# Optimization experiments

Measured on AMD Instinct MI355X. Metric: run time of the kernel, lower is better.

Reference implementation:

```python
import jax, jax.numpy as jnp
import numpy as np
from math import log2, floor

B, N, DIM = 2, 2048, 2048
HEADS, DIM_HEAD, FF_MULT = 16, 128, 4
RMS_EPS = 1e-8


def _get_slopes(heads):
    def pow2_slopes(n):
        start = 2 ** (-2 ** (-(log2(n) - 3)))
        return [start * start ** i for i in range(n)]
    if log2(heads).is_integer():
        return pow2_slopes(heads)
    closest = 2 ** floor(log2(heads))
    return pow2_slopes(closest) + pow2_slopes(2 * closest)[0::2][: heads - closest]


def setup_inputs() -> dict:
    key = jax.random.key(0)
    ks = jax.random.split(key, 5)
    std = 0.02
    return {
        "x": jax.random.normal(ks[0], (B, N, DIM), dtype=jnp.float32),
        "g": jnp.ones((DIM,), dtype=jnp.float32),
        "w_qkv": jax.random.normal(ks[1], (DIM, DIM + DIM_HEAD), dtype=jnp.float32) * std,
        "w_attn_out": jax.random.normal(ks[2], (DIM, DIM), dtype=jnp.float32) * std,
        "w_ff1": jax.random.normal(ks[3], (DIM, 2 * FF_MULT * DIM), dtype=jnp.float32) * std,
        "w_ff2": jax.random.normal(ks[4], (FF_MULT * DIM, DIM), dtype=jnp.float32) * std,
    }


def reference(x, g, w_qkv, w_attn_out, w_ff1, w_ff2):
    b, n, dim = x.shape
    # RMSNorm: x / clamp(||x|| * dim^-0.5, eps) * g
    norm = jnp.linalg.norm(x, axis=-1, keepdims=True) * (dim ** -0.5)
    xn = x / jnp.maximum(norm, RMS_EPS) * g

    # Parallel SwiGLU FFN branch (shares normed input with attention)
    h = xn @ w_ff1                       # [b, n, 2*ff_mult*dim]
    val, gate = jnp.split(h, 2, axis=-1)
    ff_out = (jax.nn.silu(gate) * val) @ w_ff2  # [b, n, dim]

    # Multi-query attention: single dim_head-wide kv shared as K and V
    qkv = xn @ w_qkv                     # [b, n, dim + dim_head]
    q, kv = qkv[..., :dim], qkv[..., dim:]
    q = q.reshape(b, n, HEADS, DIM_HEAD) * (DIM_HEAD ** -0.5)
    sim = jnp.einsum('bihd,bjd->bhij', q, kv)  # [b, h, n, n]

    # ALiBi bias: -|j - i| * slope_h
    slopes = jnp.asarray(_get_slopes(HEADS), dtype=sim.dtype)[:, None, None]
    pos = jnp.arange(n)
    bias = -jnp.abs(pos[None, None, :] - pos[None, :, None]).astype(sim.dtype) * slopes
    sim = sim + bias

    # Causal mask (strict upper triangle masked)
    causal = jnp.triu(jnp.ones((n, n), dtype=bool), 1)
    neg = jnp.asarray(jnp.finfo(sim.dtype).max, sim.dtype)
    sim = jnp.where(causal, -neg, sim)

    attn = jax.nn.softmax(sim, axis=-1)
    out = jnp.einsum('bhij,bjd->bhid', attn, kv)     # [b, h, n, dim_head]
    out = out.transpose(0, 2, 1, 3).reshape(b, n, dim)
    return out @ w_attn_out + ff_out
```

## Files before the change

### kernel.cpp

```cpp
#include <hip/hip_runtime.h>
#include <stdint.h>

typedef unsigned short u16;
typedef __attribute__((ext_vector_type(8))) short bf16x8;
typedef __attribute__((ext_vector_type(4))) float f32x4;
typedef __attribute__((ext_vector_type(8))) unsigned short us8;
typedef __attribute__((ext_vector_type(4))) float fvec4;

#define BATCH 2
#define SEQ   2048
#define DIMM  2048
#define NH    16
#define DH    128
#define ROWS  (BATCH*SEQ)
#define QKVN  (DIMM + DH)
#define FFH   8192
#define LOG2E 1.44269504088896340736f

static __device__ __forceinline__ u16 f2bf(float x) {
  union { float f; uint32_t u; } v; v.f = x;
  uint32_t r = (v.u + 0x7fffu + ((v.u >> 16) & 1u)) >> 16;
  return (u16)r;
}

static __device__ __forceinline__ float fast_exp2(float x) {
  float r; asm("v_exp_f32 %0, %1" : "=v"(r) : "v"(x)); return r;
}

static __device__ __forceinline__ void gld_lds16(const void* g, void* l) {
  __builtin_amdgcn_global_load_lds(
      (const __attribute__((address_space(1))) uint32_t*)g,
      (__attribute__((address_space(3))) uint32_t*)l, 16, 0, 0);
}

__global__ __launch_bounds__(256)
void rmsnorm_k(const float* __restrict__ x, const float* __restrict__ g, u16* __restrict__ xn) {
  const int row = blockIdx.x;
  const float* xr = x + (size_t)row * DIMM;
  const int off = threadIdx.x * 8;
  fvec4 a = *(const fvec4*)(xr + off);
  fvec4 b = *(const fvec4*)(xr + off + 4);
  float ss = a[0]*a[0]+a[1]*a[1]+a[2]*a[2]+a[3]*a[3]
           + b[0]*b[0]+b[1]*b[1]+b[2]*b[2]+b[3]*b[3];
  #pragma unroll
  for (int m = 32; m >= 1; m >>= 1) ss += __shfl_xor(ss, m);
  __shared__ float red[4];
  if ((threadIdx.x & 63) == 0) red[threadIdx.x >> 6] = ss;
  __syncthreads();
  float tot = red[0] + red[1] + red[2] + red[3];
  float inv = 1.0f / fmaxf(sqrtf(tot * (1.0f / DIMM)), 1e-8f);
  fvec4 ga = *(const fvec4*)(g + off);
  fvec4 gb = *(const fvec4*)(g + off + 4);
  us8 o;
  #pragma unroll
  for (int i = 0; i < 4; i++) { o[i] = f2bf(a[i]*inv*ga[i]); o[4+i] = f2bf(b[i]*inv*gb[i]); }
  *(us8*)(xn + (size_t)row * DIMM + off) = o;
}

template<typename TIN>
__global__ __launch_bounds__(256)
void transpose_to_bf16(const TIN* __restrict__ in, u16* __restrict__ out, int R, int C) {
  __shared__ u16 tile[64 * 65];
  const int r0 = blockIdx.y * 64, c0 = blockIdx.x * 64;
  const int tr = threadIdx.x >> 2;
  const int tc = (threadIdx.x & 3) * 16;
  const TIN* ip = in + (size_t)(r0 + tr) * C + c0 + tc;
  u16 tmp[16];
  #pragma unroll
  for (int i = 0; i < 16; i++) {
    if constexpr (sizeof(TIN) == 4) tmp[i] = f2bf(((const float*)ip)[i]);
    else                            tmp[i] = ((const u16*)ip)[i];
  }
  #pragma unroll
  for (int i = 0; i < 16; i++) tile[tr * 65 + tc + i] = tmp[i];
  __syncthreads();
  const int oc  = c0 + tr;
  const int orr = (threadIdx.x & 3) * 16;
  us8 v0, v1;
  #pragma unroll
  for (int i = 0; i < 8; i++) v0[i] = tile[(orr + i) * 65 + tr];
  #pragma unroll
  for (int i = 0; i < 8; i++) v1[i] = tile[(orr + 8 + i) * 65 + tr];
  u16* op = out + (size_t)oc * R + r0 + orr;
  *(us8*)op = v0;
  *(us8*)(op + 8) = v1;
}

__global__ __launch_bounds__(256, 2)
void gemm1_fused(const u16* __restrict__ A, const u16* __restrict__ BTff1,
                 const u16* __restrict__ BTqkv, u16* __restrict__ FF,
                 u16* __restrict__ outQ, u16* __restrict__ outKV) {
  __shared__ __align__(16) u16 lA[128 * 32];
  __shared__ __align__(16) u16 lB[128 * 32];
  const int tid = threadIdx.x;
  const int wave = tid >> 6, lane = tid & 63;
  const int lid = lane & 15, quad = lane >> 4;
  const int wm = wave >> 1, wn = wave & 1;
  const int row0 = blockIdx.y * 128;
  const bool isff = (blockIdx.x < 128);
  const int n0   = blockIdx.x * 64;
  const int col0 = (blockIdx.x - 128) * 128;
  const int K = DIMM;

  f32x4 acc[4][4];
  #pragma unroll
  for (int i = 0; i < 4; i++)
    #pragma unroll
    for (int j = 0; j < 4; j++) { acc[i][j][0]=0.f; acc[i][j][1]=0.f; acc[i][j][2]=0.f; acc[i][j][3]=0.f; }

  const int rA0 = wave * 32;
  const int rsub = lane >> 2;
  const int cl = lane & 3;

  int rbrow[4];
  #pragma unroll
  for (int in = 0; in < 4; in++)
    rbrow[in] = isff ? ((in < 2) ? (wn * 32 + in * 16) : (64 + wn * 32 + (in - 2) * 16))
                     : (wn * 64 + in * 16);

  for (int k0 = 0; k0 < K; k0 += 32) {
    #pragma unroll
    for (int h2 = 0; h2 < 2; ++h2) {
      int rloc = rA0 + h2 * 16 + rsub;
      int gc = cl ^ ((rloc >> 1) & 3);
      int grow = isff ? ((rloc < 64) ? (n0 + rloc) : (FFH + n0 + rloc - 64))
                      : (col0 + rloc);
      gld_lds16(A + (size_t)(row0 + rloc) * K + k0 + gc * 8, lA + (rA0 + h2 * 16) * 32);
      gld_lds16((isff ? BTff1 : BTqkv) + (size_t)grow * K + k0 + gc * 8,
                lB + (rA0 + h2 * 16) * 32);
    }
    __syncthreads();
    bf16x8 af[4], bfr[4];
    #pragma unroll
    for (int i = 0; i < 4; i++) {
      int r  = wm * 64 + i * 16 + lid;
      af[i]  = *(const bf16x8*)(lA + r * 32 + (quad ^ ((r >> 1) & 3)) * 8);
      int rb = rbrow[i] + lid;
      bfr[i] = *(const bf16x8*)(lB + rb * 32 + (quad ^ ((rb >> 1) & 3)) * 8);
    }
    #pragma unroll
    for (int im = 0; im < 4; im++)
      #pragma unroll
      for (int in = 0; in < 4; in++)
        acc[im][in] = __builtin_amdgcn_mfma_f32_16x16x32_bf16(af[im], bfr[in], acc[im][in], 0, 0, 0);
    __syncthreads();
  }

  if (isff) {
    #pragma unroll
    for (int im = 0; im < 4; im++)
      #pragma unroll
      for (int in = 0; in < 2; in++) {
        int col = n0 + wn * 32 + in * 16 + lid;
        int rbase = row0 + wm * 64 + im * 16 + quad * 4;
        #pragma unroll
        for (int rg = 0; rg < 4; rg++) {
          float vv = acc[im][in][rg];
          float gg = acc[im][in + 2][rg];
          float sig = 1.0f / (1.0f + fast_exp2(-gg * LOG2E));
          FF[(size_t)(rbase + rg) * FFH + col] = f2bf(vv * gg * sig);
        }
      }
  } else {
    #pragma unroll
    for (int im = 0; im < 4; im++)
      #pragma unroll
      for (int in = 0; in < 4; in++) {
        int col = col0 + wn * 64 + in * 16 + lid;
        int rbase = row0 + wm * 64 + im * 16 + quad * 4;
        #pragma unroll
        for (int rg = 0; rg < 4; rg++) {
          float v = acc[im][in][rg];
          int row = rbase + rg;
          if (col < DIMM) outQ[(size_t)row * DIMM + col] = f2bf(v);
          else            outKV[(size_t)row * DH + (col - DIMM)] = f2bf(v);
        }
      }
  }
}

__global__ __launch_bounds__(256, 2)
void gemm2_fused(const u16* __restrict__ Aff, const u16* __restrict__ Aat,
                 const u16* __restrict__ BTff2, const u16* __restrict__ BTat,
                 float* __restrict__ out) {
  __shared__ __align__(16) u16 lA[128 * 32];
  __shared__ __align__(16) u16 lB[128 * 32];
  const int tid = threadIdx.x;
  const int wave = tid >> 6, lane = tid & 63;
  const int lid = lane & 15, quad = lane >> 4;
  const int wm = wave >> 1, wn = wave & 1;
  const int row0 = blockIdx.y * 128;
  const int col0 = blockIdx.x * 128;
  f32x4 acc[4][4];
  #pragma unroll
  for (int i = 0; i < 4; i++)
    #pragma unroll
    for (int j = 0; j < 4; j++) { acc[i][j][0]=0.f; acc[i][j][1]=0.f; acc[i][j][2]=0.f; acc[i][j][3]=0.f; }

  const int rA0 = wave * 32;
  const int rsub = lane >> 2;
  const int cl = lane & 3;

  for (int k0 = 0; k0 < FFH + DIMM; k0 += 32) {
    const bool p1 = (k0 < FFH);
    const u16* Ab = p1 ? Aff : Aat;
    const u16* Bb = p1 ? BTff2 : BTat;
    const int kk = p1 ? k0 : (k0 - FFH);
    const int ld = p1 ? FFH : DIMM;
    #pragma unroll
    for (int h2 = 0; h2 < 2; ++h2) {
      int rloc = rA0 + h2 * 16 + rsub;
      int gc = cl ^ ((rloc >> 1) & 3);
      gld_lds16(Ab + (size_t)(row0 + rloc) * ld + kk + gc * 8, lA + (rA0 + h2 * 16) * 32);
      gld_lds16(Bb + (size_t)(col0 + rloc) * ld + kk + gc * 8, lB + (rA0 + h2 * 16) * 32);
    }
    __syncthreads();
    bf16x8 af[4], bfr[4];
    #pragma unroll
    for (int i = 0; i < 4; i++) {
      int r  = wm * 64 + i * 16 + lid;
      af[i]  = *(const bf16x8*)(lA + r * 32 + (quad ^ ((r >> 1) & 3)) * 8);
      int rb = wn * 64 + i * 16 + lid;
      bfr[i] = *(const bf16x8*)(lB + rb * 32 + (quad ^ ((rb >> 1) & 3)) * 8);
    }
    #pragma unroll
    for (int im = 0; im < 4; im++)
      #pragma unroll
      for (int in = 0; in < 4; in++)
        acc[im][in] = __builtin_amdgcn_mfma_f32_16x16x32_bf16(af[im], bfr[in], acc[im][in], 0, 0, 0);
    __syncthreads();
  }

  #pragma unroll
  for (int im = 0; im < 4; im++)
    #pragma unroll
    for (int in = 0; in < 4; in++) {
      int col = col0 + wn * 64 + in * 16 + lid;
      int rbase = row0 + wm * 64 + im * 16 + quad * 4;
      #pragma unroll
      for (int rg = 0; rg < 4; rg++)
        out[(size_t)(rbase + rg) * DIMM + col] = acc[im][in][rg];
    }
}

__global__ __launch_bounds__(256, 1)
void attn_k2(const u16* __restrict__ qws, const u16* __restrict__ kvws,
             const u16* __restrict__ kvt, u16* __restrict__ attnws) {
  __shared__ __align__(16) u16 kvls[128 * 128];
  __shared__ __align__(16) u16 kvtls[128 * 128];
  __shared__ __align__(16) u16 plds[4][32][136];
  const int tid = threadIdx.x;
  const int wave = tid >> 6, lane = tid & 63;
  const int lid = lane & 15, quad = lane >> 4;
  const int hb = blockIdx.y;
  const int h = hb & (NH - 1), b = hb >> 4;
  const int pair = blockIdx.x;
  const float slope2 = fast_exp2(-0.5f * (float)(h + 1)) * LOG2E;
  const float scale2 = 0.08838834764831845f * LOG2E;
  const float NEG = -__builtin_inff();

  const u16* kvb  = kvws + (size_t)b * SEQ * DH;
  const u16* kvtb = kvt  + (size_t)b * DH * SEQ;

  #pragma unroll 1
  for (int tt = 0; tt < 2; tt++) {
    const int T = tt ? (15 - pair) : pair;
    const int rw = T * 128 + wave * 32;

    bf16x8 qf[2][4];
    #pragma unroll
    for (int ig = 0; ig < 2; ig++)
      #pragma unroll
      for (int ks = 0; ks < 4; ks++)
        qf[ig][ks] = *(const bf16x8*)(qws + (size_t)(b * SEQ + rw + ig * 16 + lid) * DIMM
                                       + h * DH + ks * 32 + quad * 8);
    float srow2[2][4];
    #pragma unroll
    for (int ig = 0; ig < 2; ig++)
      #pragma unroll
      for (int rg = 0; rg < 4; rg++)
        srow2[ig][rg] = slope2 * (float)(rw + ig * 16 + quad * 4 + rg);

    f32x4 o[2][8];
    #pragma unroll
    for (int ig = 0; ig < 2; ig++)
      #pragma unroll
      for (int nd = 0; nd < 8; nd++) { o[ig][nd][0]=0.f; o[ig][nd][1]=0.f; o[ig][nd][2]=0.f; o[ig][nd][3]=0.f; }
    float m2[2][4], l[2][4];
    #pragma unroll
    for (int ig = 0; ig < 2; ig++)
      #pragma unroll
      for (int rg = 0; rg < 4; rg++) { m2[ig][rg] = NEG; l[ig][rg] = 0.f; }

    const int njt = T + 1;
    #pragma unroll 1
    for (int jt = 0; jt < njt; jt++) {
      const int j0 = jt * 128;
      __syncthreads();
      {
        const int c = lane & 15;
        const int r4 = lane >> 4;
        #pragma unroll
        for (int it = 0; it < 8; it++) {
          const int r = wave * 32 + it * 4 + r4;
          const int gc = c ^ (r & 15);
          gld_lds16(kvb  + (size_t)(j0 + r) * DH + gc * 8,        kvls  + (wave * 32 + it * 4) * 128);
          gld_lds16(kvtb + (size_t)r * SEQ + j0 + gc * 8,         kvtls + (wave * 32 + it * 4) * 128);
        }
      }
      __syncthreads();

      const int rhi = rw + 31;
      const int nbmax = min(8, ((rhi - j0) >> 4) + 1);
      const int ks2max = (nbmax + 1) >> 1;

      float pvv[2][8][4];
      float mt[2][4];
      #pragma unroll
      for (int ig = 0; ig < 2; ig++)
        #pragma unroll
        for (int rg = 0; rg < 4; rg++) mt[ig][rg] = NEG;

      #pragma unroll
      for (int nb = 0; nb < 8; nb++) {
        if (nb < nbmax) {
          bf16x8 bk[4];
          #pragma unroll
          for (int ks = 0; ks < 4; ks++)
            bk[ks] = *(const bf16x8*)(kvls + (nb * 16 + lid) * 128 + (((ks * 4 + quad) ^ lid) << 3));
          f32x4 s0, s1;
          s0[0]=0.f;s0[1]=0.f;s0[2]=0.f;s0[3]=0.f;
          s1[0]=0.f;s1[1]=0.f;s1[2]=0.f;s1[3]=0.f;
          #pragma unroll
          for (int ks = 0; ks < 4; ks++) {
            s0 = __builtin_amdgcn_mfma_f32_16x16x32_bf16(qf[0][ks], bk[ks], s0, 0, 0, 0);
            s1 = __builtin_amdgcn_mfma_f32_16x16x32_bf16(qf[1][ks], bk[ks], s1, 0, 0, 0);
          }
          const int jl = j0 + nb * 16 + lid;
          const float sj = slope2 * (float)jl;
          #pragma unroll
          for (int rg = 0; rg < 4; rg++) {
            const int row0r = rw + quad * 4 + rg;
            float e0 = fmaf(s0[rg], scale2, sj) - srow2[0][rg];
            e0 = (jl <= row0r) ? e0 : NEG;
            pvv[0][nb][rg] = e0;
            mt[0][rg] = fmaxf(mt[0][rg], e0);
            float e1 = fmaf(s1[rg], scale2, sj) - srow2[1][rg];
            e1 = (jl <= row0r + 16) ? e1 : NEG;
            pvv[1][nb][rg] = e1;
            mt[1][rg] = fmaxf(mt[1][rg], e1);
          }
        }
      }

      float alpha[2][4];
      #pragma unroll
      for (int ig = 0; ig < 2; ig++)
        #pragma unroll
        for (int rg = 0; rg < 4; rg++) {
          float m = mt[ig][rg];
          m = fmaxf(m, __shfl_xor(m, 1));
          m = fmaxf(m, __shfl_xor(m, 2));
          m = fmaxf(m, __shfl_xor(m, 4));
          m = fmaxf(m, __shfl_xor(m, 8));
          float mn = fmaxf(m2[ig][rg], m);
          alpha[ig][rg] = fast_exp2(m2[ig][rg] - mn);
          m2[ig][rg] = mn;
        }

      float rs[2][4];
      #pragma unroll
      for (int ig = 0; ig < 2; ig++)
        #pragma unroll
        for (int rg = 0; rg < 4; rg++) rs[ig][rg] = 0.f;
      #pragma unroll
      for (int nb = 0; nb < 8; nb++) {
        if (nb < nbmax) {
          #pragma unroll
          for (int ig = 0; ig < 2; ig++)
            #pragma unroll
            for (int rg = 0; rg < 4; rg++) {
              float p = fast_exp2(pvv[ig][nb][rg] - m2[ig][rg]);
              rs[ig][rg] += p;
              plds[wave][ig * 16 + quad * 4 + rg][nb * 16 + lid] = f2bf(p);
            }
        }
      }
      if (nbmax & 1) {
        #pragma unroll
        for (int ig = 0; ig < 2; ig++)
          #pragma unroll
          for (int rg = 0; rg < 4; rg++)
            plds[wave][ig * 16 + quad * 4 + rg][nbmax * 16 + lid] = 0;
      }

      #pragma unroll
      for (int ig = 0; ig < 2; ig++)
        #pragma unroll
        for (int rg = 0; rg < 4; rg++) {
          float r = rs[ig][rg];
          r += __shfl_xor(r, 1);
          r += __shfl_xor(r, 2);
          r += __shfl_xor(r, 4);
          r += __shfl_xor(r, 8);
          l[ig][rg] = l[ig][rg] * alpha[ig][rg] + r;
        }
      #pragma unroll
      for (int ig = 0; ig < 2; ig++)
        #pragma unroll
        for (int nd = 0; nd < 8; nd++)
          #pragma unroll
          for (int rg = 0; rg < 4; rg++) o[ig][nd][rg] *= alpha[ig][rg];

      asm volatile("s_waitcnt lgkmcnt(0)" ::: "memory");
      #pragma unroll
      for (int ks2 = 0; ks2 < 4; ks2++) {
        if (ks2 < ks2max) {
          bf16x8 pa0 = *(const bf16x8*)&plds[wave][lid][ks2 * 32 + quad * 8];
          bf16x8 pa1 = *(const bf16x8*)&plds[wave][16 + lid][ks2 * 32 + quad * 8];
          #pragma unroll
          for (int nd = 0; nd < 8; nd++) {
            bf16x8 bv = *(const bf16x8*)(kvtls + (nd * 16 + lid) * 128 + (((ks2 * 4 + quad) ^ lid) << 3));
            o[0][nd] = __builtin_amdgcn_mfma_f32_16x16x32_bf16(pa0, bv, o[0][nd], 0, 0, 0);
            o[1][nd] = __builtin_amdgcn_mfma_f32_16x16x32_bf16(pa1, bv, o[1][nd], 0, 0, 0);
          }
        }
      }
    }

    #pragma unroll
    for (int ig = 0; ig < 2; ig++) {
      float inv[4];
      #pragma unroll
      for (int rg = 0; rg < 4; rg++) inv[rg] = 1.0f / l[ig][rg];
      #pragma unroll
      for (int nd = 0; nd < 8; nd++)
        #pragma unroll
        for (int rg = 0; rg < 4; rg++) {
          int row = rw + ig * 16 + quad * 4 + rg;
          attnws[(size_t)(b * SEQ + row) * DIMM + h * DH + nd * 16 + lid] =
              f2bf(o[ig][nd][rg] * inv[rg]);
        }
    }
  }
}

extern "C" void kernel_launch(void* const* d_in, const int* in_sizes, int n_in,
                              void* d_out, int out_size, void* d_ws, size_t ws_size,
                              hipStream_t stream) {
  (void)in_sizes; (void)n_in; (void)out_size; (void)ws_size;
  const float* x     = (const float*)d_in[0];
  const float* g     = (const float*)d_in[1];
  const float* w_qkv = (const float*)d_in[2];
  const float* w_ao  = (const float*)d_in[3];
  const float* w_ff1 = (const float*)d_in[4];
  const float* w_ff2 = (const float*)d_in[5];
  float* out = (float*)d_out;

  u16* ws = (u16*)d_ws;
  u16* xn     = ws;
  u16* wTqkv  = xn     + 8388608;
  u16* wTattn = wTqkv  + 4456448;
  u16* wTff1  = wTattn + 4194304;
  u16* wTff2  = wTff1  + 33554432;
  u16* ffin   = wTff2  + 16777216;
  u16* qws    = ffin   + 33554432;
  u16* kvws   = qws    + 8388608;
  u16* kvtws  = kvws   + 524288;
  u16* attnws = kvtws  + 524288;

  transpose_to_bf16<float><<<dim3(QKVN/64, DIMM/64), 256, 0, stream>>>(w_qkv, wTqkv, DIMM, QKVN);
  transpose_to_bf16<float><<<dim3(DIMM/64, DIMM/64), 256, 0, stream>>>(w_ao, wTattn, DIMM, DIMM);
  transpose_to_bf16<float><<<dim3((2*FFH)/64, DIMM/64), 256, 0, stream>>>(w_ff1, wTff1, DIMM, 2*FFH);
  transpose_to_bf16<float><<<dim3(DIMM/64, FFH/64), 256, 0, stream>>>(w_ff2, wTff2, FFH, DIMM);

  rmsnorm_k<<<ROWS, 256, 0, stream>>>(x, g, xn);

  gemm1_fused<<<dim3(FFH/64 + QKVN/128, ROWS/128), 256, 0, stream>>>(
      xn, wTff1, wTqkv, ffin, qws, kvws);

  transpose_to_bf16<u16><<<dim3(DH/64, SEQ/64), 256, 0, stream>>>(kvws, kvtws, SEQ, DH);
  transpose_to_bf16<u16><<<dim3(DH/64, SEQ/64), 256, 0, stream>>>(kvws + (size_t)SEQ*DH, kvtws + (size_t)DH*SEQ, SEQ, DH);

  attn_k2<<<dim3(8, NH*BATCH), 256, 0, stream>>>(qws, kvws, kvtws, attnws);

  gemm2_fused<<<dim3(DIMM/128, ROWS/128), 256, 0, stream>>>(
      ffin, attnws, wTff2, wTattn, out);
}
```

Before: 1.086 ms.

## Share one LDS buffer for K and V^T in attention; swizzle gemm1 block order

The attention kernel now holds a single 128x128 LDS tile. It loads K, computes scores, then overwrites the tile with V^T before the PV MFMAs. This cuts LDS use so launch bounds can allow two blocks per CU, at the cost of extra barriers and serialising the V^T load after QK. Separately, gemm1 switches to a 1D grid with grouped block remapping: consecutive blocks share a column group and walk down rows, aiming for better L2 reuse of weight tiles.

```diff
diff --git a/kernel.cpp b/kernel.cpp
--- a/kernel.cpp
+++ b/kernel.cpp
@@ -92,14 +92,19 @@
                  u16* __restrict__ outQ, u16* __restrict__ outKV) {
   __shared__ __align__(16) u16 lA[128 * 32];
   __shared__ __align__(16) u16 lB[128 * 32];
+  const int cid = blockIdx.x;
+  const int group = cid >> 9;
+  const int within = cid & 511;
+  const int bx = group * 16 + (within >> 5);
+  const int by = within & 31;
   const int tid = threadIdx.x;
   const int wave = tid >> 6, lane = tid & 63;
   const int lid = lane & 15, quad = lane >> 4;
   const int wm = wave >> 1, wn = wave & 1;
-  const int row0 = blockIdx.y * 128;
-  const bool isff = (blockIdx.x < 128);
-  const int n0   = blockIdx.x * 64;
-  const int col0 = (blockIdx.x - 128) * 128;
+  const int row0 = by * 128;
+  const bool isff = (bx < 128);
+  const int n0   = bx * 64;
+  const int col0 = (bx - 128) * 128;
   const int K = DIMM;
 
   f32x4 acc[4][4];
@@ -243,11 +248,10 @@
     }
 }
 
-__global__ __launch_bounds__(256, 1)
+__global__ __launch_bounds__(256, 2)
 void attn_k2(const u16* __restrict__ qws, const u16* __restrict__ kvws,
              const u16* __restrict__ kvt, u16* __restrict__ attnws) {
-  __shared__ __align__(16) u16 kvls[128 * 128];
-  __shared__ __align__(16) u16 kvtls[128 * 128];
+  __shared__ __align__(16) u16 kls[128 * 128];
   __shared__ __align__(16) u16 plds[4][32][136];
   const int tid = threadIdx.x;
   const int wave = tid >> 6, lane = tid & 63;
@@ -296,17 +300,15 @@
     #pragma unroll 1
     for (int jt = 0; jt < njt; jt++) {
       const int j0 = jt * 128;
+      const int c = lane & 15;
+      const int r4 = lane >> 4;
+
       __syncthreads();
-      {
-        const int c = lane & 15;
-        const int r4 = lane >> 4;
-        #pragma unroll
-        for (int it = 0; it < 8; it++) {
-          const int r = wave * 32 + it * 4 + r4;
-          const int gc = c ^ (r & 15);
-          gld_lds16(kvb  + (size_t)(j0 + r) * DH + gc * 8,        kvls  + (wave * 32 + it * 4) * 128);
-          gld_lds16(kvtb + (size_t)r * SEQ + j0 + gc * 8,         kvtls + (wave * 32 + it * 4) * 128);
-        }
+      #pragma unroll
+      for (int it = 0; it < 8; it++) {
+        const int r = wave * 32 + it * 4 + r4;
+        const int gc = c ^ (r & 15);
+        gld_lds16(kvb + (size_t)(j0 + r) * DH + gc * 8, kls + (wave * 32 + it * 4) * 128);
       }
       __syncthreads();
 
@@ -327,7 +329,7 @@
           bf16x8 bk[4];
           #pragma unroll
           for (int ks = 0; ks < 4; ks++)
-            bk[ks] = *(const bf16x8*)(kvls + (nb * 16 + lid) * 128 + (((ks * 4 + quad) ^ lid) << 3));
+            bk[ks] = *(const bf16x8*)(kls + (nb * 16 + lid) * 128 + (((ks * 4 + quad) ^ lid) << 3));
           f32x4 s0, s1;
           s0[0]=0.f;s0[1]=0.f;s0[2]=0.f;s0[3]=0.f;
           s1[0]=0.f;s1[1]=0.f;s1[2]=0.f;s1[3]=0.f;
@@ -353,6 +355,14 @@
         }
       }
 
+      __syncthreads();
+      #pragma unroll
+      for (int it = 0; it < 8; it++) {
+        const int r = wave * 32 + it * 4 + r4;
+        const int gc = c ^ (r & 15);
+        gld_lds16(kvtb + (size_t)r * SEQ + j0 + gc * 8, kls + (wave * 32 + it * 4) * 128);
+      }
+
       float alpha[2][4];
       #pragma unroll
       for (int ig = 0; ig < 2; ig++)
@@ -412,7 +422,7 @@
           #pragma unroll
           for (int rg = 0; rg < 4; rg++) o[ig][nd][rg] *= alpha[ig][rg];
 
-      asm volatile("s_waitcnt lgkmcnt(0)" ::: "memory");
+      __syncthreads();
       #pragma unroll
       for (int ks2 = 0; ks2 < 4; ks2++) {
         if (ks2 < ks2max) {
@@ -420,7 +430,7 @@
           bf16x8 pa1 = *(const bf16x8*)&plds[wave][16 + lid][ks2 * 32 + quad * 8];
           #pragma unroll
           for (int nd = 0; nd < 8; nd++) {
-            bf16x8 bv = *(const bf16x8*)(kvtls + (nd * 16 + lid) * 128 + (((ks2 * 4 + quad) ^ lid) << 3));
+            bf16x8 bv = *(const bf16x8*)(kls + (nd * 16 + lid) * 128 + (((ks2 * 4 + quad) ^ lid) << 3));
             o[0][nd] = __builtin_amdgcn_mfma_f32_16x16x32_bf16(pa0, bv, o[0][nd], 0, 0, 0);
             o[1][nd] = __builtin_amdgcn_mfma_f32_16x16x32_bf16(pa1, bv, o[1][nd], 0, 0, 0);
           }
@@ -476,7 +486,7 @@
 
   rmsnorm_k<<<ROWS, 256, 0, stream>>>(x, g, xn);
 
-  gemm1_fused<<<dim3(FFH/64 + QKVN/128, ROWS/128), 256, 0, stream>>>(
+  gemm1_fused<<<dim3((FFH/64 + QKVN/128) * (ROWS/128)), 256, 0, stream>>>(
       xn, wTff1, wTqkv, ffin, qws, kvws);
 
   transpose_to_bf16<u16><<<dim3(DH/64, SEQ/64), 256, 0, stream>>>(kvws, kvtws, SEQ, DH);
```

Result: slower. 1.114 ms (+2.6%).
